# Performance work log

Measured on AMD Instinct MI355X. Metric: run time of the kernel, lower is better.

Reference implementation:

```python
import jax, jax.numpy as jnp
import numpy as np

N_EMBD = 64
N_HEAD = 4
HEAD_DIM = N_EMBD // N_HEAD
EPS = 1e-5


def _layer_norm(x, g, b):
    mu = jnp.mean(x, axis=-1, keepdims=True)
    var = jnp.mean(jnp.square(x - mu), axis=-1, keepdims=True)
    return (x - mu) * jax.lax.rsqrt(var + EPS) * g + b


def setup_inputs() -> dict:
    key = jax.random.key(0)
    ks = jax.random.split(key, 8)
    B, T, C = 4096, 64, N_EMBD
    s = 0.02
    return {
        "x": jax.random.normal(ks[0], (B, T, C), dtype=jnp.float32),
        "ln1_g": jnp.ones((C,), jnp.float32),
        "ln1_b": jnp.zeros((C,), jnp.float32),
        "attn_qkv_w": s * jax.random.normal(ks[1], (C, 3 * C), jnp.float32),
        "attn_qkv_b": jnp.zeros((3 * C,), jnp.float32),
        "attn_proj_w": s * jax.random.normal(ks[2], (C, C), jnp.float32),
        "attn_proj_b": jnp.zeros((C,), jnp.float32),
        "ln2_g": jnp.ones((C,), jnp.float32),
        "ln2_b": jnp.zeros((C,), jnp.float32),
        "fc_w": s * jax.random.normal(ks[3], (C, 4 * C), jnp.float32),
        "fc_b": jnp.zeros((4 * C,), jnp.float32),
        "proj_w": s * jax.random.normal(ks[4], (4 * C, C), jnp.float32),
        "proj_b": jnp.zeros((C,), jnp.float32),
    }


def reference(x, ln1_g, ln1_b, attn_qkv_w, attn_qkv_b, attn_proj_w, attn_proj_b,
              ln2_g, ln2_b, fc_w, fc_b, proj_w, proj_b):
    B, T, C = x.shape
    # --- self-attention branch (dropout in eval mode = identity) ---
    h = _layer_norm(x, ln1_g, ln1_b)
    qkv = h @ attn_qkv_w + attn_qkv_b                      # [B,T,3C]
    q, k, v = jnp.split(qkv, 3, axis=-1)
    def heads(t):
        return t.reshape(B, T, N_HEAD, HEAD_DIM).transpose(0, 2, 1, 3)  # [B,H,T,d]
    q, k, v = heads(q), heads(k), heads(v)
    att = jnp.einsum('bhqd,bhkd->bhqk', q, k) * (1.0 / np.sqrt(HEAD_DIM))
    causal = jnp.tril(jnp.ones((T, T), bool))
    att = jnp.where(causal, att, -jnp.inf)
    att = jax.nn.softmax(att, axis=-1)
    y = jnp.einsum('bhqk,bhkd->bhqd', att, v)              # [B,H,T,d]
    y = y.transpose(0, 2, 1, 3).reshape(B, T, C)
    x = x + (y @ attn_proj_w + attn_proj_b)
    # --- MLP branch ---
    h = _layer_norm(x, ln2_g, ln2_b)
    h = jax.nn.gelu(h @ fc_w + fc_b, approximate=False)
    x = x + (h @ proj_w + proj_b)
    return x
```

## Files before the change

### kernel.cpp

```cpp
#include <hip/hip_runtime.h>
#include <hip/hip_bf16.h>

typedef short bf16x8 __attribute__((ext_vector_type(8)));
typedef float f32x4 __attribute__((ext_vector_type(4)));
typedef __hip_bfloat16 bf16;

__global__ void prep_weights(const float* __restrict__ qkv_w,
                             const float* __restrict__ proj_w,
                             const float* __restrict__ fc_w,
                             const float* __restrict__ proj2_w,
                             bf16* __restrict__ ws) {
    int i = blockIdx.x * blockDim.x + threadIdx.x;
    float v;
    if (i < 12288)      { int n = i >> 6,              k = i & 63;    v = qkv_w[k * 192 + n]; }
    else if (i < 16384) { int j = i - 12288, n = j >> 6, k = j & 63;  v = proj_w[k * 64 + n]; }
    else if (i < 32768) { int j = i - 16384, n = j >> 6, k = j & 63;  v = fc_w[k * 256 + n]; }
    else if (i < 49152) { int j = i - 32768, n = j >> 8, k = j & 255; v = proj2_w[k * 64 + n]; }
    else return;
    ws[i] = __float2bfloat16(v);
}

__global__ __launch_bounds__(256, 2)
void gpt_block(const float* __restrict__ x,
               const float* __restrict__ ln1_g, const float* __restrict__ ln1_b,
               const float* __restrict__ qkv_b, const float* __restrict__ proj_b,
               const float* __restrict__ ln2_g, const float* __restrict__ ln2_b,
               const float* __restrict__ fc_b,  const float* __restrict__ proj2_b,
               const bf16* __restrict__ ws,
               float* __restrict__ out) {
    __shared__ __align__(16) char smem[78848];
    float* xs   = (float*)smem;
    bf16*  hb   = (bf16*)(smem + 17408);
    bf16*  qkvb = (bf16*)(smem + 26624);
    bf16*  vT   = (bf16*)(smem + 44032);
    bf16*  hm   = (bf16*)(smem + 26624);
    bf16*  pb   = (bf16*)(smem + 60416);
    bf16*  yb   = (bf16*)(smem + 69632);

    const int tid = threadIdx.x;
    const int w   = tid >> 6;
    const int l   = tid & 63;
    const int lr  = l & 15;
    const int lk  = l >> 4;
    const size_t b = blockIdx.x;
    const float* xb = x + b * 4096;

    {
        const float4* src = (const float4*)xb;
        #pragma unroll
        for (int j = 0; j < 4; ++j) {
            int idx  = j * 256 + tid;
            float4 v = src[idx];
            int row  = idx >> 4;
            int col  = (idx & 15) * 4;
            *(float4*)&xs[row * 68 + col] = v;
        }
    }
    __syncthreads();

    auto layer_norm = [&](const float* g, const float* be) {
        int row = w * 16 + (l >> 2);
        int q   = l & 3;
        const float* xr = &xs[row * 68];
        float vals[16];
        float s0 = 0.f, s1 = 0.f;
        #pragma unroll
        for (int cv = 0; cv < 4; ++cv) {
            float4 v4 = *(const float4*)&xr[q * 16 + cv * 4];
            vals[cv*4+0] = v4.x; vals[cv*4+1] = v4.y; vals[cv*4+2] = v4.z; vals[cv*4+3] = v4.w;
            s0 += v4.x + v4.y + v4.z + v4.w;
            s1 += v4.x*v4.x + v4.y*v4.y + v4.z*v4.z + v4.w*v4.w;
        }
        s0 += __shfl_xor(s0, 1); s1 += __shfl_xor(s1, 1);
        s0 += __shfl_xor(s0, 2); s1 += __shfl_xor(s1, 2);
        float mu   = s0 * (1.f / 64.f);
        float var  = s1 * (1.f / 64.f) - mu * mu;
        float rstd = rsqrtf(var + 1e-5f);
        bf16 tmp[16];
        #pragma unroll
        for (int c = 0; c < 16; ++c) {
            int cc = q * 16 + c;
            tmp[c] = __float2bfloat16((vals[c] - mu) * rstd * g[cc] + be[cc]);
        }
        *(uint4*)&hb[row * 72 + q * 16]     = *(uint4*)&tmp[0];
        *(uint4*)&hb[row * 72 + q * 16 + 8] = *(uint4*)&tmp[8];
    };

    layer_norm(ln1_g, ln1_b);
    __syncthreads();

    {
        const short* wq = (const short*)ws;
        #pragma unroll
        for (int t = 0; t < 3; ++t) {
            int nt = w + t * 4;
            bf16x8 bfr[2];
            #pragma unroll
            for (int ks = 0; ks < 2; ++ks)
                bfr[ks] = *(const bf16x8*)(wq + (nt * 16 + lr) * 64 + ks * 32 + lk * 8);
            float bias = qkv_b[nt * 16 + lr];
            #pragma unroll
            for (int mt = 0; mt < 4; ++mt) {
                f32x4 acc = {};
                #pragma unroll
                for (int ks = 0; ks < 2; ++ks) {
                    bf16x8 a = *(const bf16x8*)((const short*)hb + (mt * 16 + lr) * 72 + ks * 32 + lk * 8);
                    acc = __builtin_amdgcn_mfma_f32_16x16x32_bf16(a, bfr[ks], acc, 0, 0, 0);
                }
                #pragma unroll
                for (int r = 0; r < 4; ++r) {
                    int m = mt * 16 + lk * 4 + r;
                    bf16 v = __float2bfloat16(acc[r] + bias);
                    if (t < 2) qkvb[m * 136 + t * 64 + w * 16 + lr] = v;
                    else       vT[(w * 16 + lr) * 72 + m] = v;
                }
            }
        }
    }
    __syncthreads();

    {
        #pragma unroll
        for (int h = 0; h < 4; ++h) {
            bf16x8 qa = {};
            if (lk < 2)
                qa = *(const bf16x8*)((const short*)qkvb + (w * 16 + lr) * 136 + h * 16 + lk * 8);
            f32x4 s[4];
            #pragma unroll
            for (int nt = 0; nt < 4; ++nt) {
                bf16x8 kb = {};
                if (lk < 2)
                    kb = *(const bf16x8*)((const short*)qkvb + (nt * 16 + lr) * 136 + 64 + h * 16 + lk * 8);
                f32x4 acc = {};
                s[nt] = __builtin_amdgcn_mfma_f32_16x16x32_bf16(qa, kb, acc, 0, 0, 0);
            }
            float p[4][4];
            float rmax[4] = {-1e30f, -1e30f, -1e30f, -1e30f};
            #pragma unroll
            for (int nt = 0; nt < 4; ++nt)
                #pragma unroll
                for (int r = 0; r < 4; ++r) {
                    int qq = w * 16 + lk * 4 + r;
                    int kk = nt * 16 + lr;
                    float v = (kk <= qq) ? s[nt][r] * 0.25f : -1e30f;
                    p[nt][r] = v;
                    rmax[r] = fmaxf(rmax[r], v);
                }
            #pragma unroll
            for (int r = 0; r < 4; ++r) {
                float m_ = rmax[r];
                m_ = fmaxf(m_, __shfl_xor(m_, 1));
                m_ = fmaxf(m_, __shfl_xor(m_, 2));
                m_ = fmaxf(m_, __shfl_xor(m_, 4));
                m_ = fmaxf(m_, __shfl_xor(m_, 8));
                rmax[r] = m_;
            }
            float rsum[4] = {0.f, 0.f, 0.f, 0.f};
            #pragma unroll
            for (int nt = 0; nt < 4; ++nt)
                #pragma unroll
                for (int r = 0; r < 4; ++r) {
                    float e = __expf(p[nt][r] - rmax[r]);
                    p[nt][r] = e;
                    rsum[r] += e;
                }
            #pragma unroll
            for (int r = 0; r < 4; ++r) {
                float s_ = rsum[r];
                s_ += __shfl_xor(s_, 1);
                s_ += __shfl_xor(s_, 2);
                s_ += __shfl_xor(s_, 4);
                s_ += __shfl_xor(s_, 8);
                rsum[r] = 1.f / s_;
            }
            #pragma unroll
            for (int nt = 0; nt < 4; ++nt)
                #pragma unroll
                for (int r = 0; r < 4; ++r)
                    pb[(w * 16 + lk * 4 + r) * 72 + nt * 16 + lr] = __float2bfloat16(p[nt][r] * rsum[r]);
            f32x4 y = {};
            #pragma unroll
            for (int ks = 0; ks < 2; ++ks) {
                bf16x8 a  = *(const bf16x8*)((const short*)pb + (w * 16 + lr) * 72 + ks * 32 + lk * 8);
                bf16x8 vb = *(const bf16x8*)((const short*)vT + (h * 16 + lr) * 72 + ks * 32 + lk * 8);
                y = __builtin_amdgcn_mfma_f32_16x16x32_bf16(a, vb, y, 0, 0, 0);
            }
            #pragma unroll
            for (int r = 0; r < 4; ++r)
                yb[(w * 16 + lk * 4 + r) * 72 + h * 16 + lr] = __float2bfloat16(y[r]);
        }
    }
    __syncthreads();

    {
        const short* wp = (const short*)ws + 12288;
        bf16x8 bfr[2];
        #pragma unroll
        for (int ks = 0; ks < 2; ++ks)
            bfr[ks] = *(const bf16x8*)(wp + (w * 16 + lr) * 64 + ks * 32 + lk * 8);
        float bias = proj_b[w * 16 + lr];
        #pragma unroll
        for (int mt = 0; mt < 4; ++mt) {
            f32x4 acc = {};
            #pragma unroll
            for (int ks = 0; ks < 2; ++ks) {
                bf16x8 a = *(const bf16x8*)((const short*)yb + (mt * 16 + lr) * 72 + ks * 32 + lk * 8);
                acc = __builtin_amdgcn_mfma_f32_16x16x32_bf16(a, bfr[ks], acc, 0, 0, 0);
            }
            #pragma unroll
            for (int r = 0; r < 4; ++r) {
                int row = mt * 16 + lk * 4 + r, col = w * 16 + lr;
                xs[row * 68 + col] += acc[r] + bias;
            }
        }
    }
    __syncthreads();

    layer_norm(ln2_g, ln2_b);
    __syncthreads();

    {
        const short* wf = (const short*)ws + 16384;
        #pragma unroll
        for (int t = 0; t < 4; ++t) {
            int nt = w + t * 4;
            bf16x8 bfr[2];
            #pragma unroll
            for (int ks = 0; ks < 2; ++ks)
                bfr[ks] = *(const bf16x8*)(wf + (nt * 16 + lr) * 64 + ks * 32 + lk * 8);
            float bias = fc_b[nt * 16 + lr];
            #pragma unroll
            for (int mt = 0; mt < 4; ++mt) {
                f32x4 acc = {};
                #pragma unroll
                for (int ks = 0; ks < 2; ++ks) {
                    bf16x8 a = *(const bf16x8*)((const short*)hb + (mt * 16 + lr) * 72 + ks * 32 + lk * 8);
                    acc = __builtin_amdgcn_mfma_f32_16x16x32_bf16(a, bfr[ks], acc, 0, 0, 0);
                }
                #pragma unroll
                for (int r = 0; r < 4; ++r) {
                    float v  = acc[r] + bias;
                    float ge = 0.5f * v * (1.f + erff(v * 0.70710678118f));
                    hm[(mt * 16 + lk * 4 + r) * 264 + nt * 16 + lr] = __float2bfloat16(ge);
                }
            }
        }
    }
    __syncthreads();

    {
        const short* wp2 = (const short*)ws + 32768;
        bf16x8 bfr[8];
        #pragma unroll
        for (int ks = 0; ks < 8; ++ks)
            bfr[ks] = *(const bf16x8*)(wp2 + (w * 16 + lr) * 256 + ks * 32 + lk * 8);
        float bias = proj2_b[w * 16 + lr];
        float* ob = out + b * 4096;
        #pragma unroll
        for (int mt = 0; mt < 4; ++mt) {
            f32x4 acc = {};
            #pragma unroll
            for (int ks = 0; ks < 8; ++ks) {
                bf16x8 a = *(const bf16x8*)((const short*)hm + (mt * 16 + lr) * 264 + ks * 32 + lk * 8);
                acc = __builtin_amdgcn_mfma_f32_16x16x32_bf16(a, bfr[ks], acc, 0, 0, 0);
            }
            #pragma unroll
            for (int r = 0; r < 4; ++r) {
                int row = mt * 16 + lk * 4 + r, col = w * 16 + lr;
                ob[row * 64 + col] = xs[row * 68 + col] + acc[r] + bias;
            }
        }
    }
}

extern "C" void kernel_launch(void* const* d_in, const int* in_sizes, int n_in,
                              void* d_out, int out_size, void* d_ws, size_t ws_size,
                              hipStream_t stream) {
    const float* x       = (const float*)d_in[0];
    const float* ln1_g   = (const float*)d_in[1];
    const float* ln1_b   = (const float*)d_in[2];
    const float* qkv_w   = (const float*)d_in[3];
    const float* qkv_b   = (const float*)d_in[4];
    const float* proj_w  = (const float*)d_in[5];
    const float* proj_b  = (const float*)d_in[6];
    const float* ln2_g   = (const float*)d_in[7];
    const float* ln2_b   = (const float*)d_in[8];
    const float* fc_w    = (const float*)d_in[9];
    const float* fc_b    = (const float*)d_in[10];
    const float* proj2_w = (const float*)d_in[11];
    const float* proj2_b = (const float*)d_in[12];
    bf16* ws  = (bf16*)d_ws;
    float* out = (float*)d_out;

    prep_weights<<<192, 256, 0, stream>>>(qkv_w, proj_w, fc_w, proj2_w, ws);
    gpt_block<<<4096, 256, 0, stream>>>(x, ln1_g, ln1_b, qkv_b, proj_b,
                                        ln2_g, ln2_b, fc_b, proj2_b, ws, out);
}
```

Measured before the change: 264.6 us.

## Rewrite fused GPT block with register-resident residual, transposed MFMA, and chunked MLP

Restructures the fused block kernel so the residual stream stays in registers instead of an fp32 shared-memory tile. MFMA operands are swapped so each lane owns a row, which lets layer norm and softmax reduce with cross-lane shuffles and allows vectorised bf16x4 stores. Shared memory drops from about 77KB to 35KB, and launch bounds rise to 4 blocks per CU. The MLP hidden layer is processed in two 128-wide chunks that accumulate into the second GEMM. Several other changes ride along: causal attention skips fully masked key tiles, erf GELU is replaced by a tanh-style approximation via exp, and softmax drops the max subtraction, which risks accuracy and overflow.

```diff
diff --git a/kernel.cpp b/kernel.cpp
--- a/kernel.cpp
+++ b/kernel.cpp
@@ -2,8 +2,14 @@
 #include <hip/hip_bf16.h>
 
 typedef short bf16x8 __attribute__((ext_vector_type(8)));
-typedef float f32x4 __attribute__((ext_vector_type(4)));
+typedef short bf16x4 __attribute__((ext_vector_type(4)));
+typedef float f32x4  __attribute__((ext_vector_type(4)));
 typedef __hip_bfloat16 bf16;
+
+static __device__ __forceinline__ short f2bf(float x) {
+    bf16 t = __float2bfloat16(x);
+    return *reinterpret_cast<short*>(&t);
+}
 
 __global__ void prep_weights(const float* __restrict__ qkv_w,
                              const float* __restrict__ proj_w,
@@ -20,7 +26,7 @@
     ws[i] = __float2bfloat16(v);
 }
 
-__global__ __launch_bounds__(256, 2)
+__global__ __launch_bounds__(256, 4)
 void gpt_block(const float* __restrict__ x,
                const float* __restrict__ ln1_g, const float* __restrict__ ln1_b,
                const float* __restrict__ qkv_b, const float* __restrict__ proj_b,
@@ -28,247 +34,245 @@
                const float* __restrict__ fc_b,  const float* __restrict__ proj2_b,
                const bf16* __restrict__ ws,
                float* __restrict__ out) {
-    __shared__ __align__(16) char smem[78848];
-    float* xs   = (float*)smem;
-    bf16*  hb   = (bf16*)(smem + 17408);
-    bf16*  qkvb = (bf16*)(smem + 26624);
-    bf16*  vT   = (bf16*)(smem + 44032);
-    bf16*  hm   = (bf16*)(smem + 26624);
-    bf16*  pb   = (bf16*)(smem + 60416);
-    bf16*  yb   = (bf16*)(smem + 69632);
+    __shared__ __align__(16) char smem[35840];
+    bf16* hb = (bf16*)smem;
+    bf16* pb = hb;
+    bf16* qk = (bf16*)(smem + 9216);
+    bf16* vT = (bf16*)(smem + 26624);
+    bf16* hm = (bf16*)(smem + 9216);
 
     const int tid = threadIdx.x;
     const int w   = tid >> 6;
     const int l   = tid & 63;
     const int lr  = l & 15;
     const int lk  = l >> 4;
+    const int row = w * 16 + lr;
     const size_t b = blockIdx.x;
-    const float* xb = x + b * 4096;
-
-    {
-        const float4* src = (const float4*)xb;
-        #pragma unroll
-        for (int j = 0; j < 4; ++j) {
-            int idx  = j * 256 + tid;
-            float4 v = src[idx];
-            int row  = idx >> 4;
-            int col  = (idx & 15) * 4;
-            *(float4*)&xs[row * 68 + col] = v;
-        }
-    }
-    __syncthreads();
-
-    auto layer_norm = [&](const float* g, const float* be) {
-        int row = w * 16 + (l >> 2);
-        int q   = l & 3;
-        const float* xr = &xs[row * 68];
-        float vals[16];
+
+    f32x4 xr[4];
+    {
+        const float* xb = x + b * 4096;
+        #pragma unroll
+        for (int nt = 0; nt < 4; ++nt)
+            xr[nt] = *(const f32x4*)&xb[row * 64 + nt * 16 + lk * 4];
+    }
+
+    auto ln = [&](const float* g, const float* be) {
         float s0 = 0.f, s1 = 0.f;
         #pragma unroll
-        for (int cv = 0; cv < 4; ++cv) {
-            float4 v4 = *(const float4*)&xr[q * 16 + cv * 4];
-            vals[cv*4+0] = v4.x; vals[cv*4+1] = v4.y; vals[cv*4+2] = v4.z; vals[cv*4+3] = v4.w;
-            s0 += v4.x + v4.y + v4.z + v4.w;
-            s1 += v4.x*v4.x + v4.y*v4.y + v4.z*v4.z + v4.w*v4.w;
-        }
-        s0 += __shfl_xor(s0, 1); s1 += __shfl_xor(s1, 1);
-        s0 += __shfl_xor(s0, 2); s1 += __shfl_xor(s1, 2);
+        for (int nt = 0; nt < 4; ++nt)
+            #pragma unroll
+            for (int r = 0; r < 4; ++r) { float v = xr[nt][r]; s0 += v; s1 += v * v; }
+        s0 += __shfl_xor(s0, 16); s1 += __shfl_xor(s1, 16);
+        s0 += __shfl_xor(s0, 32); s1 += __shfl_xor(s1, 32);
         float mu   = s0 * (1.f / 64.f);
         float var  = s1 * (1.f / 64.f) - mu * mu;
         float rstd = rsqrtf(var + 1e-5f);
-        bf16 tmp[16];
-        #pragma unroll
-        for (int c = 0; c < 16; ++c) {
-            int cc = q * 16 + c;
-            tmp[c] = __float2bfloat16((vals[c] - mu) * rstd * g[cc] + be[cc]);
-        }
-        *(uint4*)&hb[row * 72 + q * 16]     = *(uint4*)&tmp[0];
-        *(uint4*)&hb[row * 72 + q * 16 + 8] = *(uint4*)&tmp[8];
+        #pragma unroll
+        for (int nt = 0; nt < 4; ++nt) {
+            f32x4 g4 = ((const f32x4*)g)[nt * 4 + lk];
+            f32x4 b4 = ((const f32x4*)be)[nt * 4 + lk];
+            bf16x4 o;
+            #pragma unroll
+            for (int r = 0; r < 4; ++r)
+                o[r] = f2bf((xr[nt][r] - mu) * rstd * g4[r] + b4[r]);
+            *(bf16x4*)&hb[row * 72 + nt * 16 + lk * 4] = o;
+        }
     };
 
-    layer_norm(ln1_g, ln1_b);
+    ln(ln1_g, ln1_b);
     __syncthreads();
 
     {
-        const short* wq = (const short*)ws;
-        #pragma unroll
-        for (int t = 0; t < 3; ++t) {
-            int nt = w + t * 4;
-            bf16x8 bfr[2];
+        const short* wsb = (const short*)ws;
+        bf16x8 hbf[4][2];
+        #pragma unroll
+        for (int mt = 0; mt < 4; ++mt)
             #pragma unroll
             for (int ks = 0; ks < 2; ++ks)
-                bfr[ks] = *(const bf16x8*)(wq + (nt * 16 + lr) * 64 + ks * 32 + lk * 8);
-            float bias = qkv_b[nt * 16 + lr];
-            #pragma unroll
-            for (int mt = 0; mt < 4; ++mt) {
-                f32x4 acc = {};
-                #pragma unroll
-                for (int ks = 0; ks < 2; ++ks) {
-                    bf16x8 a = *(const bf16x8*)((const short*)hb + (mt * 16 + lr) * 72 + ks * 32 + lk * 8);
-                    acc = __builtin_amdgcn_mfma_f32_16x16x32_bf16(a, bfr[ks], acc, 0, 0, 0);
-                }
-                #pragma unroll
-                for (int r = 0; r < 4; ++r) {
-                    int m = mt * 16 + lk * 4 + r;
-                    bf16 v = __float2bfloat16(acc[r] + bias);
-                    if (t < 2) qkvb[m * 136 + t * 64 + w * 16 + lr] = v;
-                    else       vT[(w * 16 + lr) * 72 + m] = v;
-                }
-            }
-        }
-    }
-    __syncthreads();
-
-    {
-        #pragma unroll
-        for (int h = 0; h < 4; ++h) {
-            bf16x8 qa = {};
-            if (lk < 2)
-                qa = *(const bf16x8*)((const short*)qkvb + (w * 16 + lr) * 136 + h * 16 + lk * 8);
-            f32x4 s[4];
-            #pragma unroll
-            for (int nt = 0; nt < 4; ++nt) {
-                bf16x8 kb = {};
-                if (lk < 2)
-                    kb = *(const bf16x8*)((const short*)qkvb + (nt * 16 + lr) * 136 + 64 + h * 16 + lk * 8);
-                f32x4 acc = {};
-                s[nt] = __builtin_amdgcn_mfma_f32_16x16x32_bf16(qa, kb, acc, 0, 0, 0);
-            }
-            float p[4][4];
-            float rmax[4] = {-1e30f, -1e30f, -1e30f, -1e30f};
-            #pragma unroll
-            for (int nt = 0; nt < 4; ++nt)
-                #pragma unroll
-                for (int r = 0; r < 4; ++r) {
-                    int qq = w * 16 + lk * 4 + r;
-                    int kk = nt * 16 + lr;
-                    float v = (kk <= qq) ? s[nt][r] * 0.25f : -1e30f;
-                    p[nt][r] = v;
-                    rmax[r] = fmaxf(rmax[r], v);
-                }
-            #pragma unroll
-            for (int r = 0; r < 4; ++r) {
-                float m_ = rmax[r];
-                m_ = fmaxf(m_, __shfl_xor(m_, 1));
-                m_ = fmaxf(m_, __shfl_xor(m_, 2));
-                m_ = fmaxf(m_, __shfl_xor(m_, 4));
-                m_ = fmaxf(m_, __shfl_xor(m_, 8));
-                rmax[r] = m_;
-            }
-            float rsum[4] = {0.f, 0.f, 0.f, 0.f};
-            #pragma unroll
-            for (int nt = 0; nt < 4; ++nt)
-                #pragma unroll
-                for (int r = 0; r < 4; ++r) {
-                    float e = __expf(p[nt][r] - rmax[r]);
-                    p[nt][r] = e;
-                    rsum[r] += e;
-                }
-            #pragma unroll
-            for (int r = 0; r < 4; ++r) {
-                float s_ = rsum[r];
-                s_ += __shfl_xor(s_, 1);
-                s_ += __shfl_xor(s_, 2);
-                s_ += __shfl_xor(s_, 4);
-                s_ += __shfl_xor(s_, 8);
-                rsum[r] = 1.f / s_;
-            }
-            #pragma unroll
-            for (int nt = 0; nt < 4; ++nt)
-                #pragma unroll
-                for (int r = 0; r < 4; ++r)
-                    pb[(w * 16 + lk * 4 + r) * 72 + nt * 16 + lr] = __float2bfloat16(p[nt][r] * rsum[r]);
-            f32x4 y = {};
-            #pragma unroll
-            for (int ks = 0; ks < 2; ++ks) {
-                bf16x8 a  = *(const bf16x8*)((const short*)pb + (w * 16 + lr) * 72 + ks * 32 + lk * 8);
-                bf16x8 vb = *(const bf16x8*)((const short*)vT + (h * 16 + lr) * 72 + ks * 32 + lk * 8);
-                y = __builtin_amdgcn_mfma_f32_16x16x32_bf16(a, vb, y, 0, 0, 0);
-            }
-            #pragma unroll
-            for (int r = 0; r < 4; ++r)
-                yb[(w * 16 + lk * 4 + r) * 72 + h * 16 + lr] = __float2bfloat16(y[r]);
-        }
-    }
-    __syncthreads();
-
-    {
-        const short* wp = (const short*)ws + 12288;
-        bf16x8 bfr[2];
-        #pragma unroll
-        for (int ks = 0; ks < 2; ++ks)
-            bfr[ks] = *(const bf16x8*)(wp + (w * 16 + lr) * 64 + ks * 32 + lk * 8);
-        float bias = proj_b[w * 16 + lr];
+                hbf[mt][ks] = *(const bf16x8*)((const short*)hb + (mt * 16 + lr) * 72 + ks * 32 + lk * 8);
+
+        bf16x8 aq[2], ak[2], bv[2];
+        #pragma unroll
+        for (int ks = 0; ks < 2; ++ks) {
+            aq[ks] = *(const bf16x8*)(wsb + (w * 16 + lr) * 64        + ks * 32 + lk * 8);
+            ak[ks] = *(const bf16x8*)(wsb + (64 + w * 16 + lr) * 64   + ks * 32 + lk * 8);
+            bv[ks] = *(const bf16x8*)(wsb + (128 + w * 16 + lr) * 64  + ks * 32 + lk * 8);
+        }
+        f32x4 qb = ((const f32x4*)qkv_b)[w * 4 + lk];
+        f32x4 kb = ((const f32x4*)qkv_b)[16 + w * 4 + lk];
+        float vbias = qkv_b[128 + w * 16 + lr];
+
         #pragma unroll
         for (int mt = 0; mt < 4; ++mt) {
             f32x4 acc = {};
             #pragma unroll
-            for (int ks = 0; ks < 2; ++ks) {
-                bf16x8 a = *(const bf16x8*)((const short*)yb + (mt * 16 + lr) * 72 + ks * 32 + lk * 8);
-                acc = __builtin_amdgcn_mfma_f32_16x16x32_bf16(a, bfr[ks], acc, 0, 0, 0);
-            }
-            #pragma unroll
-            for (int r = 0; r < 4; ++r) {
-                int row = mt * 16 + lk * 4 + r, col = w * 16 + lr;
-                xs[row * 68 + col] += acc[r] + bias;
-            }
-        }
-    }
-    __syncthreads();
-
-    layer_norm(ln2_g, ln2_b);
-    __syncthreads();
-
-    {
-        const short* wf = (const short*)ws + 16384;
-        #pragma unroll
-        for (int t = 0; t < 4; ++t) {
-            int nt = w + t * 4;
-            bf16x8 bfr[2];
-            #pragma unroll
             for (int ks = 0; ks < 2; ++ks)
-                bfr[ks] = *(const bf16x8*)(wf + (nt * 16 + lr) * 64 + ks * 32 + lk * 8);
-            float bias = fc_b[nt * 16 + lr];
-            #pragma unroll
-            for (int mt = 0; mt < 4; ++mt) {
-                f32x4 acc = {};
-                #pragma unroll
-                for (int ks = 0; ks < 2; ++ks) {
-                    bf16x8 a = *(const bf16x8*)((const short*)hb + (mt * 16 + lr) * 72 + ks * 32 + lk * 8);
-                    acc = __builtin_amdgcn_mfma_f32_16x16x32_bf16(a, bfr[ks], acc, 0, 0, 0);
-                }
-                #pragma unroll
-                for (int r = 0; r < 4; ++r) {
-                    float v  = acc[r] + bias;
-                    float ge = 0.5f * v * (1.f + erff(v * 0.70710678118f));
-                    hm[(mt * 16 + lk * 4 + r) * 264 + nt * 16 + lr] = __float2bfloat16(ge);
-                }
-            }
-        }
-    }
-    __syncthreads();
-
-    {
-        const short* wp2 = (const short*)ws + 32768;
-        bf16x8 bfr[8];
-        #pragma unroll
-        for (int ks = 0; ks < 8; ++ks)
-            bfr[ks] = *(const bf16x8*)(wp2 + (w * 16 + lr) * 256 + ks * 32 + lk * 8);
-        float bias = proj2_b[w * 16 + lr];
-        float* ob = out + b * 4096;
+                acc = __builtin_amdgcn_mfma_f32_16x16x32_bf16(aq[ks], hbf[mt][ks], acc, 0, 0, 0);
+            bf16x4 o;
+            #pragma unroll
+            for (int r = 0; r < 4; ++r) o[r] = f2bf(acc[r] + qb[r]);
+            *(bf16x4*)&qk[(mt * 16 + lr) * 136 + w * 16 + lk * 4] = o;
+        }
         #pragma unroll
         for (int mt = 0; mt < 4; ++mt) {
             f32x4 acc = {};
             #pragma unroll
-            for (int ks = 0; ks < 8; ++ks) {
-                bf16x8 a = *(const bf16x8*)((const short*)hm + (mt * 16 + lr) * 264 + ks * 32 + lk * 8);
-                acc = __builtin_amdgcn_mfma_f32_16x16x32_bf16(a, bfr[ks], acc, 0, 0, 0);
-            }
-            #pragma unroll
-            for (int r = 0; r < 4; ++r) {
-                int row = mt * 16 + lk * 4 + r, col = w * 16 + lr;
-                ob[row * 64 + col] = xs[row * 68 + col] + acc[r] + bias;
-            }
+            for (int ks = 0; ks < 2; ++ks)
+                acc = __builtin_amdgcn_mfma_f32_16x16x32_bf16(ak[ks], hbf[mt][ks], acc, 0, 0, 0);
+            bf16x4 o;
+            #pragma unroll
+            for (int r = 0; r < 4; ++r) o[r] = f2bf(acc[r] + kb[r]);
+            *(bf16x4*)&qk[(mt * 16 + lr) * 136 + 64 + w * 16 + lk * 4] = o;
+        }
+        #pragma unroll
+        for (int mt = 0; mt < 4; ++mt) {
+            f32x4 acc = {};
+            #pragma unroll
+            for (int ks = 0; ks < 2; ++ks)
+                acc = __builtin_amdgcn_mfma_f32_16x16x32_bf16(hbf[mt][ks], bv[ks], acc, 0, 0, 0);
+            bf16x4 o;
+            #pragma unroll
+            for (int r = 0; r < 4; ++r) o[r] = f2bf(acc[r] + vbias);
+            *(bf16x4*)&vT[(w * 16 + lr) * 72 + mt * 16 + lk * 4] = o;
+        }
+    }
+    __syncthreads();
+
+    {
+        bf16x4 z = {};
+        for (int kt = w + 1; kt < 4; ++kt)
+            *(bf16x4*)&pb[row * 72 + kt * 16 + lk * 4] = z;
+
+        #pragma unroll
+        for (int h = 0; h < 4; ++h) {
+            bf16x8 qf = {};
+            if (lk < 2)
+                qf = *(const bf16x8*)((const short*)qk + row * 136 + h * 16 + lk * 8);
+            float pr[4][4];
+            float psum = 0.f;
+            for (int kt = 0; kt <= w; ++kt) {
+                bf16x8 kf = {};
+                if (lk < 2)
+                    kf = *(const bf16x8*)((const short*)qk + (kt * 16 + lr) * 136 + 64 + h * 16 + lk * 8);
+                f32x4 acc = {};
+                f32x4 sv = __builtin_amdgcn_mfma_f32_16x16x32_bf16(kf, qf, acc, 0, 0, 0);
+                #pragma unroll
+                for (int r = 0; r < 4; ++r) {
+                    float s = sv[r] * 0.25f;
+                    if (kt == w && (4 * lk + r) > lr) s = -1e30f;
+                    float e = __expf(s);
+                    pr[kt][r] = e; psum += e;
+                }
+            }
+            psum += __shfl_xor(psum, 16);
+            psum += __shfl_xor(psum, 32);
+            float rinv = __builtin_amdgcn_rcpf(psum);
+            for (int kt = 0; kt <= w; ++kt) {
+                bf16x4 o;
+                #pragma unroll
+                for (int r = 0; r < 4; ++r) o[r] = f2bf(pr[kt][r] * rinv);
+                *(bf16x4*)&pb[row * 72 + kt * 16 + lk * 4] = o;
+            }
+            f32x4 y = {};
+            #pragma unroll
+            for (int ks = 0; ks < 2; ++ks) {
+                bf16x8 vf = *(const bf16x8*)((const short*)vT + (h * 16 + lr) * 72 + ks * 32 + lk * 8);
+                bf16x8 pf = *(const bf16x8*)((const short*)pb + row * 72 + ks * 32 + lk * 8);
+                y = __builtin_amdgcn_mfma_f32_16x16x32_bf16(vf, pf, y, 0, 0, 0);
+            }
+            bf16x4 o;
+            #pragma unroll
+            for (int r = 0; r < 4; ++r) o[r] = f2bf(y[r]);
+            *(bf16x4*)&qk[row * 136 + h * 16 + lk * 4] = o;
+        }
+    }
+
+    {
+        const short* wp = (const short*)ws + 12288;
+        bf16x8 yf[2];
+        #pragma unroll
+        for (int ks = 0; ks < 2; ++ks)
+            yf[ks] = *(const bf16x8*)((const short*)qk + row * 136 + ks * 32 + lk * 8);
+        #pragma unroll
+        for (int nt = 0; nt < 4; ++nt) {
+            f32x4 acc = {};
+            #pragma unroll
+            for (int ks = 0; ks < 2; ++ks) {
+                bf16x8 a = *(const bf16x8*)(wp + (nt * 16 + lr) * 64 + ks * 32 + lk * 8);
+                acc = __builtin_amdgcn_mfma_f32_16x16x32_bf16(a, yf[ks], acc, 0, 0, 0);
+            }
+            f32x4 pb4 = ((const f32x4*)proj_b)[nt * 4 + lk];
+            #pragma unroll
+            for (int r = 0; r < 4; ++r) xr[nt][r] += acc[r] + pb4[r];
+        }
+    }
+    __syncthreads();
+
+    ln(ln2_g, ln2_b);
+    __syncthreads();
+
+    f32x4 acc2[4] = {f32x4{}, f32x4{}, f32x4{}, f32x4{}};
+    {
+        const short* wf = (const short*)ws + 16384;
+        const short* w2 = (const short*)ws + 32768;
+        for (int H = 0; H < 2; ++H) {
+            #pragma unroll
+            for (int u = 0; u < 2; ++u) {
+                int lt = w + u * 4;
+                int gt = H * 8 + lt;
+                bf16x8 af[2];
+                #pragma unroll
+                for (int ks = 0; ks < 2; ++ks)
+                    af[ks] = *(const bf16x8*)(wf + (gt * 16 + lr) * 64 + ks * 32 + lk * 8);
+                f32x4 fb = ((const f32x4*)fc_b)[gt * 4 + lk];
+                #pragma unroll
+                for (int mt = 0; mt < 4; ++mt) {
+                    f32x4 acc = {};
+                    #pragma unroll
+                    for (int ks = 0; ks < 2; ++ks) {
+                        bf16x8 hf = *(const bf16x8*)((const short*)hb + (mt * 16 + lr) * 72 + ks * 32 + lk * 8);
+                        acc = __builtin_amdgcn_mfma_f32_16x16x32_bf16(af[ks], hf, acc, 0, 0, 0);
+                    }
+                    bf16x4 o;
+                    #pragma unroll
+                    for (int r = 0; r < 4; ++r) {
+                        float v = acc[r] + fb[r];
+                        float u_ = v * (0.7978845608f + 0.0356774081f * v * v);
+                        u_ = fminf(u_, 8.f);
+                        float e = __expf(2.f * u_);
+                        float ge = v * e * __builtin_amdgcn_rcpf(1.f + e);
+                        o[r] = f2bf(ge);
+                    }
+                    *(bf16x4*)&hm[(mt * 16 + lr) * 136 + lt * 16 + lk * 4] = o;
+                }
+            }
+            __syncthreads();
+            bf16x8 hf4[4];
+            #pragma unroll
+            for (int ks = 0; ks < 4; ++ks)
+                hf4[ks] = *(const bf16x8*)((const short*)hm + row * 136 + ks * 32 + lk * 8);
+            #pragma unroll
+            for (int nt = 0; nt < 4; ++nt) {
+                #pragma unroll
+                for (int ks = 0; ks < 4; ++ks) {
+                    bf16x8 a = *(const bf16x8*)(w2 + (nt * 16 + lr) * 256 + H * 128 + ks * 32 + lk * 8);
+                    acc2[nt] = __builtin_amdgcn_mfma_f32_16x16x32_bf16(a, hf4[ks], acc2[nt], 0, 0, 0);
+                }
+            }
+            if (H == 0) __syncthreads();
+        }
+    }
+
+    {
+        float* ob = out + b * 4096;
+        #pragma unroll
+        for (int nt = 0; nt < 4; ++nt) {
+            f32x4 b2 = ((const f32x4*)proj2_b)[nt * 4 + lk];
+            f32x4 o;
+            #pragma unroll
+            for (int r = 0; r < 4; ++r) o[r] = xr[nt][r] + acc2[nt][r] + b2[r];
+            *(f32x4*)&ob[row * 64 + nt * 16 + lk * 4] = o;
         }
     }
 }
@@ -289,7 +293,7 @@
     const float* fc_b    = (const float*)d_in[10];
     const float* proj2_w = (const float*)d_in[11];
     const float* proj2_b = (const float*)d_in[12];
-    bf16* ws  = (bf16*)d_ws;
+    bf16* ws   = (bf16*)d_ws;
     float* out = (float*)d_out;
 
     prep_weights<<<192, 256, 0, stream>>>(qkv_w, proj_w, fc_w, proj2_w, ws);
```

Result: faster. 244.1 us (-7.7%).
